# Kernel tuning notes

Measured on AMD Instinct MI355X. Metric: run time of the kernel, lower is better.

## Reference

```python
import jax, jax.numpy as jnp
import numpy as np

N = 100_000      # nodes
E = 3_200_000    # edges (avg degree 32)
HID = 64         # hid_dim == in_dim
T = 4            # S2V propagation rounds


def setup_inputs() -> dict:
    key = jax.random.key(0)
    ks = jax.random.split(key, 10)
    s = lambda fan: 1.0 / np.sqrt(fan)
    return {
        "x": jax.random.normal(ks[0], (N, HID), jnp.float32),
        "x_tag": jax.random.uniform(ks[1], (N,), jnp.float32),
        "edge_attr": jax.random.uniform(ks[2], (E, 1), jnp.float32),
        "edge_index": jax.random.randint(ks[3], (2, E), 0, N, dtype=jnp.int32),
        # per-layer bias-free Linear weights (stored as [in, out])
        "W1": jax.random.normal(ks[4], (T, HID), jnp.float32),            # lin1: 1 -> hid
        "W2": jax.random.normal(ks[5], (T, HID, HID), jnp.float32) * s(HID),  # lin2: in -> hid
        "W4": jax.random.normal(ks[6], (T, HID), jnp.float32),            # lin4: 1 -> hid
        "W5": jax.random.normal(ks[7], (2 * HID, 1), jnp.float32) * s(2 * HID),  # lin5
        "W6": jax.random.normal(ks[8], (HID, HID), jnp.float32) * s(HID),  # lin6
        "W7": jax.random.normal(ks[9], (HID, HID), jnp.float32) * s(HID),  # lin7
    }


def reference(x, x_tag, edge_attr, edge_index, W1, W2, W4, W5, W6, W7):
    src = edge_index[0]  # j (message source / p3 scatter target)
    dst = edge_index[1]  # i (aggregation target)
    for l in range(T):  # fixed small layer count
        p1 = x_tag[:, None] * W1[l][None, :]                        # lin1(x_tag)  [N,HID]
        e = jax.nn.relu(edge_attr * W4[l][None, :])                  # relu(lin4(edge_attr)) [E,HID]
        aggr = jax.ops.segment_sum(x[src], dst, num_segments=N)     # add-aggregate x_j at i
        p2 = aggr @ W2[l]                                            # lin2(aggr_out)
        p3 = jax.ops.segment_sum(e, src, num_segments=N)             # scatter_add at edge_index[0]
        x = jax.nn.relu(p1 + p2 + p3)
    graph_pool = jnp.sum(x, axis=0, keepdims=True) @ W6              # [1,HID]
    nodes_vec = x @ W7                                               # [N,HID]
    cat = jnp.concatenate(
        [jnp.broadcast_to(graph_pool, (x.shape[0], graph_pool.shape[1])), nodes_vec], axis=1
    )
    Q = jax.nn.relu(cat) @ W5                                        # [N,1]
    return Q
```

## Files before the change

### kernel.cpp

```cpp
#include <hip/hip_runtime.h>

constexpr int NN  = 100000;
constexpr int NE  = 3200000;
constexpr int HID = 64;
constexpr int TL  = 4;

constexpr int BIN_SHIFT = 9;
constexpr int BIN_NODES = 1 << BIN_SHIFT;
constexpr int NBINS     = (NN + BIN_NODES - 1) / BIN_NODES;
constexpr int BINCAP    = 18944;
constexpr int TILE_E    = 2048;

typedef unsigned short ushort_t;
typedef unsigned int uint_t;
typedef __attribute__((ext_vector_type(8))) short bf16x8;
typedef __attribute__((ext_vector_type(4))) float f32x4;

__device__ __forceinline__ ushort_t f2b(float f) {
  uint_t u = __float_as_uint(f);
  u += 0x7fff + ((u >> 16) & 1);
  return (ushort_t)(u >> 16);
}
__device__ __forceinline__ float b2f(ushort_t h) {
  return __uint_as_float(((uint_t)h) << 16);
}

__global__ __launch_bounds__(256) void escatter_kernel(
    const int* __restrict__ ei, const float* __restrict__ ea,
    int* __restrict__ bincursor, uint_t* __restrict__ gbin,
    int* __restrict__ bincursor2, uint_t* __restrict__ gbin2) {
  __shared__ int hist1[256], hist2[256];
  __shared__ int base1[NBINS], base2[NBINS];
  __shared__ int offs1[NBINS], offs2[NBINS];
  __shared__ uint_t srec[TILE_E];
  __shared__ int    sdst[TILE_E];
  int tid = threadIdx.x;
  int tb = blockIdx.x * TILE_E;
  hist1[tid] = 0; hist2[tid] = 0;
  __syncthreads();
  uint_t rec1[8], rec2[8]; int bn1[8], bn2[8], rk1[8], rk2[8];
  #pragma unroll
  for (int j = 0; j < 8; ++j) {
    int e = tb + tid + j * 256;
    bn1[j] = -1; bn2[j] = -1;
    rk1[j] = 0; rk2[j] = 0; rec1[j] = 0; rec2[j] = 0;
    if (e < NE) {
      int s = ei[e];
      int d = ei[NE + e];
      uint_t q = (uint_t)(int)(ea[e] * 8388608.0f);
      bn1[j] = d >> BIN_SHIFT;
      rec1[j] = ((uint_t)s << BIN_SHIFT) | (uint_t)(d & (BIN_NODES - 1));
      rk1[j] = atomicAdd(&hist1[bn1[j]], 1);
      bn2[j] = s >> BIN_SHIFT;
      rec2[j] = (q << BIN_SHIFT) | (uint_t)(s & (BIN_NODES - 1));
      rk2[j] = atomicAdd(&hist2[bn2[j]], 1);
    }
  }
  __syncthreads();
  int c1 = hist1[tid], c2 = hist2[tid];
  for (int o = 1; o < 256; o <<= 1) {
    int a1 = (tid >= o) ? hist1[tid - o] : 0;
    int a2 = (tid >= o) ? hist2[tid - o] : 0;
    __syncthreads();
    hist1[tid] += a1; hist2[tid] += a2;
    __syncthreads();
  }
  if (tid < NBINS) {
    offs1[tid] = hist1[tid] - c1;
    offs2[tid] = hist2[tid] - c2;
    base1[tid] = c1 ? atomicAdd(&bincursor[tid], c1) : 0;
    base2[tid] = c2 ? atomicAdd(&bincursor2[tid], c2) : 0;
  }
  __syncthreads();
  int total1 = hist1[NBINS - 1];
  int total2 = hist2[NBINS - 1];
  #pragma unroll
  for (int j = 0; j < 8; ++j) {
    if (bn1[j] >= 0) {
      int p = offs1[bn1[j]] + rk1[j];
      int gp = base1[bn1[j]] + rk1[j];
      srec[p] = rec1[j];
      sdst[p] = (gp < BINCAP) ? (bn1[j] * BINCAP + gp) : -1;
    }
  }
  __syncthreads();
  for (int t = tid; t < total1; t += 256) {
    int g = sdst[t];
    if (g >= 0) gbin[g] = srec[t];
  }
  __syncthreads();
  #pragma unroll
  for (int j = 0; j < 8; ++j) {
    if (bn2[j] >= 0) {
      int p = offs2[bn2[j]] + rk2[j];
      int gp = base2[bn2[j]] + rk2[j];
      srec[p] = rec2[j];
      sdst[p] = (gp < BINCAP) ? (bn2[j] * BINCAP + gp) : -1;
    }
  }
  __syncthreads();
  for (int t = tid; t < total2; t += 256) {
    int g = sdst[t];
    if (g >= 0) gbin2[g] = srec[t];
  }
}

__global__ __launch_bounds__(256) void binscatter_kernel(
    const int* __restrict__ ei, int* __restrict__ bincursor,
    uint_t* __restrict__ gbin) {
  __shared__ int hist[NBINS];
  __shared__ int base[NBINS];
  int tid = threadIdx.x;
  int ntiles = (NE + TILE_E - 1) / TILE_E;
  for (int tile = blockIdx.x; tile < ntiles; tile += gridDim.x) {
    int tb = tile * TILE_E;
    for (int i = tid; i < NBINS; i += 256) hist[i] = 0;
    __syncthreads();
    uint_t rec[8]; int bn[8]; int rk[8];
    #pragma unroll
    for (int j = 0; j < 8; ++j) {
      int e = tb + tid + j * 256;
      bn[j] = -1; rk[j] = 0; rec[j] = 0;
      if (e < NE) {
        int s = ei[e];
        int d = ei[NE + e];
        bn[j] = d >> BIN_SHIFT;
        rec[j] = ((uint_t)s << BIN_SHIFT) | (uint_t)(d & (BIN_NODES - 1));
        rk[j] = atomicAdd(&hist[bn[j]], 1);
      }
    }
    __syncthreads();
    for (int i = tid; i < NBINS; i += 256) {
      int c = hist[i];
      base[i] = c ? atomicAdd(&bincursor[i], c) : 0;
    }
    __syncthreads();
    #pragma unroll
    for (int j = 0; j < 8; ++j) {
      if (bn[j] >= 0) {
        int pos = base[bn[j]] + rk[j];
        if (pos < BINCAP) gbin[(size_t)bn[j] * BINCAP + pos] = rec[j];
      }
    }
    __syncthreads();
  }
}

__global__ __launch_bounds__(256) void sbinscatter_kernel(
    const int* __restrict__ ei, const float* __restrict__ ea,
    int* __restrict__ bincursor2, uint_t* __restrict__ gbin) {
  __shared__ int hist[NBINS];
  __shared__ int base[NBINS];
  int tid = threadIdx.x;
  int ntiles = (NE + TILE_E - 1) / TILE_E;
  for (int tile = blockIdx.x; tile < ntiles; tile += gridDim.x) {
    int tb = tile * TILE_E;
    for (int i = tid; i < NBINS; i += 256) hist[i] = 0;
    __syncthreads();
    uint_t rec[8]; int bn[8]; int rk[8];
    #pragma unroll
    for (int j = 0; j < 8; ++j) {
      int e = tb + tid + j * 256;
      bn[j] = -1; rk[j] = 0; rec[j] = 0;
      if (e < NE) {
        int s = ei[e];
        uint_t q = (uint_t)(int)(ea[e] * 8388608.0f);
        bn[j] = s >> BIN_SHIFT;
        rec[j] = (q << BIN_SHIFT) | (uint_t)(s & (BIN_NODES - 1));
        rk[j] = atomicAdd(&hist[bn[j]], 1);
      }
    }
    __syncthreads();
    for (int i = tid; i < NBINS; i += 256) {
      int c = hist[i];
      base[i] = c ? atomicAdd(&bincursor2[i], c) : 0;
    }
    __syncthreads();
    #pragma unroll
    for (int j = 0; j < 8; ++j) {
      if (bn[j] >= 0) {
        int pos = base[bn[j]] + rk[j];
        if (pos < BINCAP) gbin[(size_t)bn[j] * BINCAP + pos] = rec[j];
      }
    }
    __syncthreads();
  }
}

__global__ __launch_bounds__(256) void bucket_kernel(
    const uint_t* __restrict__ gbin, const int* __restrict__ bincursor,
    int* __restrict__ colidx, int* __restrict__ cnt, int cap) {
  __shared__ int cur[BIN_NODES];
  int b = blockIdx.x;
  int tid = threadIdx.x;
  for (int i = tid; i < BIN_NODES; i += 256) cur[i] = 0;
  __syncthreads();
  int cb = min(bincursor[b], BINCAP);
  const uint_t* g = gbin + (size_t)b * BINCAP;
  for (int i = tid; i < cb; i += 256) {
    uint_t r = g[i];
    int dl = (int)(r & (BIN_NODES - 1));
    int src = (int)(r >> BIN_SHIFT);
    int pos = atomicAdd(&cur[dl], 1);
    int n = (b << BIN_SHIFT) + dl;
    if (pos < cap) colidx[(size_t)n * cap + pos] = src;
  }
  __syncthreads();
  for (int i = tid; i < BIN_NODES; i += 256) {
    int n = (b << BIN_SHIFT) + i;
    if (n < NN) cnt[n] = min(cur[i], cap);
  }
  for (int gsl = tid; gsl < BIN_NODES * 64; gsl += 256) {
    int i = gsl >> 6;
    int s = gsl & 63;
    int n = (b << BIN_SHIFT) + i;
    if (n < NN && s < 48 && s >= cur[i]) colidx[(size_t)n * cap + s] = NN;
  }
}

__global__ __launch_bounds__(256) void s3bucket_kernel(
    const uint_t* __restrict__ gbin, const int* __restrict__ bincursor2,
    int* __restrict__ s3i) {
  __shared__ int acc[BIN_NODES];
  int b = blockIdx.x;
  int tid = threadIdx.x;
  for (int i = tid; i < BIN_NODES; i += 256) acc[i] = 0;
  __syncthreads();
  int cb = min(bincursor2[b], BINCAP);
  const uint_t* g = gbin + (size_t)b * BINCAP;
  for (int i = tid; i < cb; i += 256) {
    uint_t r = g[i];
    atomicAdd(&acc[r & (BIN_NODES - 1)], (int)(r >> BIN_SHIFT));
  }
  __syncthreads();
  for (int i = tid; i < BIN_NODES; i += 256) {
    int n = (b << BIN_SHIFT) + i;
    if (n < NN) s3i[n] = acc[i];
  }
}

__global__ void conv_kernel(const float* __restrict__ x, ushort_t* __restrict__ xb) {
  int i = blockIdx.x * blockDim.x + threadIdx.x;
  if (i * 4 >= NN * HID) return;
  const float4 v = *reinterpret_cast<const float4*>(&x[i * 4]);
  ushort4 o;
  o.x = f2b(v.x); o.y = f2b(v.y); o.z = f2b(v.z); o.w = f2b(v.w);
  *reinterpret_cast<ushort4*>(&xb[i * 4]) = o;
}

__global__ void wconv_kernel(const float* __restrict__ W2,
                             const float* __restrict__ W7,
                             ushort_t* __restrict__ w2t,
                             ushort_t* __restrict__ w7t) {
  int i = blockIdx.x * blockDim.x + threadIdx.x;
  int tot2 = TL * HID * HID;
  if (i < tot2) {
    int l = i >> 12, r = i & 4095, h = r >> 6, k = r & 63;
    w2t[i] = f2b(W2[(size_t)l * 4096 + k * 64 + h]);
  } else if (i < tot2 + HID * HID) {
    int j = i - tot2, h = j >> 6, k = j & 63;
    w7t[j] = f2b(W7[k * 64 + h]);
  }
}

__global__ __launch_bounds__(256) void dense_kernel(
    const ushort_t* __restrict__ xin, const ushort_t* __restrict__ wt,
    ushort_t* __restrict__ yout) {
  int lane = threadIdx.x & 63;
  int wv = (blockIdx.x * blockDim.x + threadIdx.x) >> 6;
  int n0 = wv * 32;
  if (n0 >= NN) return;
  int row = lane & 15;
  int ks = (lane >> 4) * 8;
  bf16x8 a0 = *(const bf16x8*)&xin[(size_t)(n0 + row) * HID + ks];
  bf16x8 a1 = *(const bf16x8*)&xin[(size_t)(n0 + row) * HID + 32 + ks];
  bf16x8 a2 = *(const bf16x8*)&xin[(size_t)(n0 + 16 + row) * HID + ks];
  bf16x8 a3 = *(const bf16x8*)&xin[(size_t)(n0 + 16 + row) * HID + 32 + ks];
  #pragma unroll
  for (int ct = 0; ct < 4; ++ct) {
    bf16x8 b0 = *(const bf16x8*)&wt[(ct * 16 + row) * HID + ks];
    bf16x8 b1 = *(const bf16x8*)&wt[(ct * 16 + row) * HID + 32 + ks];
    f32x4 acc0 = {0.f, 0.f, 0.f, 0.f};
    f32x4 acc1 = {0.f, 0.f, 0.f, 0.f};
    acc0 = __builtin_amdgcn_mfma_f32_16x16x32_bf16(a0, b0, acc0, 0, 0, 0);
    acc0 = __builtin_amdgcn_mfma_f32_16x16x32_bf16(a1, b1, acc0, 0, 0, 0);
    acc1 = __builtin_amdgcn_mfma_f32_16x16x32_bf16(a2, b0, acc1, 0, 0, 0);
    acc1 = __builtin_amdgcn_mfma_f32_16x16x32_bf16(a3, b1, acc1, 0, 0, 0);
    int rr = (lane >> 4) * 4;
    #pragma unroll
    for (int r = 0; r < 4; ++r) {
      yout[(size_t)(n0 + rr + r) * HID + ct * 16 + row] = f2b(acc0[r]);
      yout[(size_t)(n0 + 16 + rr + r) * HID + ct * 16 + row] = f2b(acc1[r]);
    }
  }
}

__global__ __launch_bounds__(256) void aggr_kernel(
    const ushort_t* __restrict__ yin, ushort_t* __restrict__ xout,
    const int* __restrict__ cnt, const int* __restrict__ colidx, int cap,
    const float* __restrict__ x_tag, const int* __restrict__ s3i,
    const float* __restrict__ W1l, const float* __restrict__ W4l) {
  int lane = threadIdx.x & 63;
  int wv = (blockIdx.x * blockDim.x + threadIdx.x) >> 6;
  int n0 = wv * 2;
  if (n0 >= NN) return;
  int half = lane >> 5;
  int n = n0 + half;
  int grp = (lane >> 3) & 3;
  int sub = lane & 7;
  const int* cl = colidx + (size_t)n * cap + grp;
  float f0 = 0.f, f1 = 0.f, f2 = 0.f, f3 = 0.f;
  float f4 = 0.f, f5 = 0.f, f6 = 0.f, f7 = 0.f;
  uint4 w[12];
  #pragma unroll
  for (int j = 0; j < 12; ++j) {
    int c = cl[j * 4];
    w[j] = *reinterpret_cast<const uint4*>(&yin[(size_t)c * HID + sub * 8]);
  }
  #pragma unroll
  for (int j = 0; j < 12; ++j) {
    f0 += __uint_as_float(w[j].x << 16);
    f1 += __uint_as_float(w[j].x & 0xffff0000u);
    f2 += __uint_as_float(w[j].y << 16);
    f3 += __uint_as_float(w[j].y & 0xffff0000u);
    f4 += __uint_as_float(w[j].z << 16);
    f5 += __uint_as_float(w[j].z & 0xffff0000u);
    f6 += __uint_as_float(w[j].w << 16);
    f7 += __uint_as_float(w[j].w & 0xffff0000u);
  }
  int deg = cnt[n];
  if (__any(deg > 48)) {
    int t2 = deg - 48;
    const int* ct2 = colidx + (size_t)n * cap + 48;
    for (int jt = 0; jt < 12; ++jt) {
      int idx = jt * 4 + grp;
      if (idx < t2) {
        int c = ct2[idx];
        uint4 ww = *reinterpret_cast<const uint4*>(&yin[(size_t)c * HID + sub * 8]);
        f0 += __uint_as_float(ww.x << 16);
        f1 += __uint_as_float(ww.x & 0xffff0000u);
        f2 += __uint_as_float(ww.y << 16);
        f3 += __uint_as_float(ww.y & 0xffff0000u);
        f4 += __uint_as_float(ww.z << 16);
        f5 += __uint_as_float(ww.z & 0xffff0000u);
        f6 += __uint_as_float(ww.w << 16);
        f7 += __uint_as_float(ww.w & 0xffff0000u);
      }
    }
  }
  #pragma unroll
  for (int m = 8; m <= 16; m <<= 1) {
    f0 += __shfl_xor(f0, m); f1 += __shfl_xor(f1, m);
    f2 += __shfl_xor(f2, m); f3 += __shfl_xor(f3, m);
    f4 += __shfl_xor(f4, m); f5 += __shfl_xor(f5, m);
    f6 += __shfl_xor(f6, m); f7 += __shfl_xor(f7, m);
  }
  float xt = x_tag[n];
  float s3f = (float)s3i[n] * 0x1p-23f;
  float4 w1a = *reinterpret_cast<const float4*>(&W1l[sub * 8]);
  float4 w1b = *reinterpret_cast<const float4*>(&W1l[sub * 8 + 4]);
  float4 w4a = *reinterpret_cast<const float4*>(&W4l[sub * 8]);
  float4 w4b = *reinterpret_cast<const float4*>(&W4l[sub * 8 + 4]);
  float o0 = fmaxf(fmaf(xt, w1a.x, fmaf(s3f, fmaxf(w4a.x, 0.f), f0)), 0.f);
  float o1 = fmaxf(fmaf(xt, w1a.y, fmaf(s3f, fmaxf(w4a.y, 0.f), f1)), 0.f);
  float o2 = fmaxf(fmaf(xt, w1a.z, fmaf(s3f, fmaxf(w4a.z, 0.f), f2)), 0.f);
  float o3 = fmaxf(fmaf(xt, w1a.w, fmaf(s3f, fmaxf(w4a.w, 0.f), f3)), 0.f);
  float o4 = fmaxf(fmaf(xt, w1b.x, fmaf(s3f, fmaxf(w4b.x, 0.f), f4)), 0.f);
  float o5 = fmaxf(fmaf(xt, w1b.y, fmaf(s3f, fmaxf(w4b.y, 0.f), f5)), 0.f);
  float o6 = fmaxf(fmaf(xt, w1b.z, fmaf(s3f, fmaxf(w4b.z, 0.f), f6)), 0.f);
  float o7 = fmaxf(fmaf(xt, w1b.w, fmaf(s3f, fmaxf(w4b.w, 0.f), f7)), 0.f);
  if (grp == 0) {
    uint4 o;
    o.x = (uint_t)f2b(o0) | ((uint_t)f2b(o1) << 16);
    o.y = (uint_t)f2b(o2) | ((uint_t)f2b(o3) << 16);
    o.z = (uint_t)f2b(o4) | ((uint_t)f2b(o5) << 16);
    o.w = (uint_t)f2b(o6) | ((uint_t)f2b(o7) << 16);
    *reinterpret_cast<uint4*>(&xout[(size_t)n * HID + sub * 8]) = o;
  }
}

__global__ __launch_bounds__(256) void qdense_kernel(
    const ushort_t* __restrict__ xin, const ushort_t* __restrict__ w7t,
    const float* __restrict__ w5hi, float* __restrict__ Qr,
    float* __restrict__ sumx) {
  __shared__ float ssum[4][HID];
  int tid = threadIdx.x;
  int lane = tid & 63;
  int wloc = tid >> 6;
  int wv = (blockIdx.x * blockDim.x + tid) >> 6;
  int n0 = wv * 16;
  bool valid = n0 < NN;
  int n0c = valid ? n0 : 0;
  int row = lane & 15;
  int g = lane >> 4;
  int ks = g * 8;
  bf16x8 a0 = *(const bf16x8*)&xin[(size_t)(n0c + row) * HID + ks];
  bf16x8 a1 = *(const bf16x8*)&xin[(size_t)(n0c + row) * HID + 32 + ks];
  float r0 = 0.f, r1 = 0.f, r2 = 0.f, r3 = 0.f;
  #pragma unroll
  for (int ct = 0; ct < 4; ++ct) {
    bf16x8 b0 = *(const bf16x8*)&w7t[(ct * 16 + row) * HID + ks];
    bf16x8 b1 = *(const bf16x8*)&w7t[(ct * 16 + row) * HID + 32 + ks];
    f32x4 acc = {0.f, 0.f, 0.f, 0.f};
    acc = __builtin_amdgcn_mfma_f32_16x16x32_bf16(a0, b0, acc, 0, 0, 0);
    acc = __builtin_amdgcn_mfma_f32_16x16x32_bf16(a1, b1, acc, 0, 0, 0);
    float w5 = w5hi[ct * 16 + row];
    r0 += fmaxf(acc[0], 0.f) * w5;
    r1 += fmaxf(acc[1], 0.f) * w5;
    r2 += fmaxf(acc[2], 0.f) * w5;
    r3 += fmaxf(acc[3], 0.f) * w5;
  }
  #pragma unroll
  for (int m = 1; m <= 8; m <<= 1) {
    r0 += __shfl_xor(r0, m); r1 += __shfl_xor(r1, m);
    r2 += __shfl_xor(r2, m); r3 += __shfl_xor(r3, m);
  }
  if (valid && row == 0) {
    int rb = n0 + g * 4;
    Qr[rb + 0] = r0; Qr[rb + 1] = r1; Qr[rb + 2] = r2; Qr[rb + 3] = r3;
  }
  float c[16];
  #pragma unroll
  for (int e = 0; e < 8; ++e) {
    c[e]     = valid ? b2f((ushort_t)a0[e]) : 0.f;
    c[8 + e] = valid ? b2f((ushort_t)a1[e]) : 0.f;
  }
  #pragma unroll
  for (int m = 1; m <= 8; m <<= 1) {
    #pragma unroll
    for (int e = 0; e < 16; ++e) c[e] += __shfl_xor(c[e], m);
  }
  if (row == 0) {
    #pragma unroll
    for (int e = 0; e < 8; ++e) {
      ssum[wloc][ks + e] = c[e];
      ssum[wloc][32 + ks + e] = c[8 + e];
    }
  }
  __syncthreads();
  if (tid < HID) {
    float s = ssum[0][tid] + ssum[1][tid] + ssum[2][tid] + ssum[3][tid];
    atomicAdd(&sumx[tid], s);
  }
}

__global__ void pool_kernel(const float* __restrict__ sumx, const float* __restrict__ W6,
                            const float* __restrict__ W5, float* __restrict__ c0) {
  int lane = threadIdx.x & 63;
  float sv = sumx[lane];
  float gp = 0.f;
  #pragma unroll
  for (int k = 0; k < HID; ++k) {
    float a = __int_as_float(__builtin_amdgcn_readlane(__float_as_int(sv), k));
    gp = fmaf(a, W6[k * HID + lane], gp);
  }
  float r = fmaxf(gp, 0.f) * W5[lane];
  #pragma unroll
  for (int m = 32; m >= 1; m >>= 1) r += __shfl_xor(r, m);
  if (lane == 0) *c0 = r;
}

__global__ void qfix_kernel(float* __restrict__ Q, const float* __restrict__ c0) {
  int i = blockIdx.x * blockDim.x + threadIdx.x;
  if (i < NN) Q[i] += *c0;
}

extern "C" void kernel_launch(void* const* d_in, const int* in_sizes, int n_in,
                              void* d_out, int out_size, void* d_ws, size_t ws_size,
                              hipStream_t stream) {
  const float* x         = (const float*)d_in[0];
  const float* x_tag     = (const float*)d_in[1];
  const float* edge_attr = (const float*)d_in[2];
  const int*   edge_index= (const int*)d_in[3];
  const float* W1        = (const float*)d_in[4];
  const float* W2        = (const float*)d_in[5];
  const float* W4        = (const float*)d_in[6];
  const float* W5        = (const float*)d_in[7];
  const float* W6        = (const float*)d_in[8];
  const float* W7        = (const float*)d_in[9];
  float* Q = (float*)d_out;

  const int QBLOCKS = ((NN / 16) * 64 + 255) / 256;
  const int NTILES  = (NE + TILE_E - 1) / TILE_E;

  char* ws = (char*)d_ws;
  size_t off = 0;
  auto alloc = [&](size_t bytes) -> void* {
    void* p = ws + off;
    off = (off + bytes + 255) & ~(size_t)255;
    return p;
  };
  int*      bincursor  = (int*)alloc(NBINS * 4);
  int*      bincursor2 = (int*)alloc(NBINS * 4);
  float*    sumx       = (float*)alloc(HID * 4);
  size_t zero_bytes = off;
  int*      s3i    = (int*)alloc(NN * 4);
  int*      cnt    = (int*)alloc(NN * 4);
  float*    c0     = (float*)alloc(4);
  ushort_t* xb0    = (ushort_t*)alloc((size_t)NN * HID * 2);
  ushort_t* xb1    = (ushort_t*)alloc((size_t)NN * HID * 2);
  ushort_t* ybuf   = (ushort_t*)alloc((size_t)(NN + 1) * HID * 2);
  ushort_t* w2t    = (ushort_t*)alloc((size_t)TL * HID * HID * 2);
  ushort_t* w7t    = (ushort_t*)alloc((size_t)HID * HID * 2);
  uint_t*   gbin   = (uint_t*)alloc((size_t)NBINS * BINCAP * 4);

  size_t off_nog2 = off;
  uint_t* gbin2 = (uint_t*)alloc((size_t)NBINS * BINCAP * 4);
  bool merged = true;
  {
    size_t rem = (ws_size > off) ? (ws_size - off) : 0;
    if ((int)(rem / ((size_t)NN * 4)) < 64) { merged = false; off = off_nog2; }
  }
  size_t rem = (ws_size > off) ? (ws_size - off) : 0;
  int cap = (int)(rem / ((size_t)NN * 4));
  if (cap > 96) cap = 96;
  if (cap < 64) cap = 64;
  int* colidx = (int*)alloc((size_t)NN * cap * 4);

  hipMemsetAsync(d_ws, 0, zero_bytes, stream);
  hipMemsetAsync(ybuf + (size_t)NN * HID, 0, HID * 2, stream);

  if (merged) {
    escatter_kernel<<<NTILES, 256, 0, stream>>>(edge_index, edge_attr,
                                                bincursor, gbin, bincursor2, gbin2);
    bucket_kernel<<<NBINS, 256, 0, stream>>>(gbin, bincursor, colidx, cnt, cap);
    s3bucket_kernel<<<NBINS, 256, 0, stream>>>(gbin2, bincursor2, s3i);
  } else {
    binscatter_kernel<<<NTILES, 256, 0, stream>>>(edge_index, bincursor, gbin);
    bucket_kernel<<<NBINS, 256, 0, stream>>>(gbin, bincursor, colidx, cnt, cap);
    sbinscatter_kernel<<<NTILES, 256, 0, stream>>>(edge_index, edge_attr, bincursor2, gbin);
    s3bucket_kernel<<<NBINS, 256, 0, stream>>>(gbin, bincursor2, s3i);
  }
  conv_kernel<<<(NN * HID / 4 + 255) / 256, 256, 0, stream>>>(x, xb0);
  wconv_kernel<<<((TL + 1) * HID * HID + 255) / 256, 256, 0, stream>>>(W2, W7, w2t, w7t);

  int ablocks = ((NN / 2) * 64 + 255) / 256;
  int dblocks = ((NN / 32) * 64 + 255) / 256;
  const ushort_t* xi = xb0;
  ushort_t* xo = xb1;
  for (int l = 0; l < TL; ++l) {
    dense_kernel<<<dblocks, 256, 0, stream>>>(xi, w2t + (size_t)l * HID * HID, ybuf);
    aggr_kernel<<<ablocks, 256, 0, stream>>>(ybuf, xo, cnt, colidx, cap,
                                             x_tag, s3i, W1 + l * HID, W4 + l * HID);
    ushort_t* tmp = (ushort_t*)xi;
    xi = xo;
    xo = (l == 0) ? xb0 : tmp;
  }

  qdense_kernel<<<QBLOCKS, 256, 0, stream>>>(xi, w7t, W5 + HID, Q, sumx);
  pool_kernel<<<1, 64, 0, stream>>>(sumx, W6, W5, c0);
  qfix_kernel<<<(NN + 255) / 256, 256, 0, stream>>>(Q, c0);
}
```

Measured before the change: 430.6 us.

## Fuse next-layer dense matmul into aggregation kernel and drop unmerged binning path

The aggregation kernel now takes the next layer's W2 and, after computing a 16-node tile of new features in shared memory, applies the 64x64 matmul with MFMA and writes the projected features directly. This removes the separate dense kernel launch per layer and the round trip of x through global memory. Only one dense launch is left, for layer 0. The escatter prefix scan now uses wave shuffles instead of a barrier-heavy shared-memory scan. The fallback non-merged binning path is removed, so gbin2 is always allocated, which reduces the room left for colidx when the workspace is small.

```diff
diff --git a/kernel.cpp b/kernel.cpp
--- a/kernel.cpp
+++ b/kernel.cpp
@@ -10,6 +10,8 @@
 constexpr int NBINS     = (NN + BIN_NODES - 1) / BIN_NODES;
 constexpr int BINCAP    = 18944;
 constexpr int TILE_E    = 2048;
+constexpr int PAD       = 48;
+constexpr int LROW      = 72;
 
 typedef unsigned short ushort_t;
 typedef unsigned int uint_t;
@@ -32,6 +34,7 @@
   __shared__ int hist1[256], hist2[256];
   __shared__ int base1[NBINS], base2[NBINS];
   __shared__ int offs1[NBINS], offs2[NBINS];
+  __shared__ int wt1[4], wt2[4];
   __shared__ uint_t srec[TILE_E];
   __shared__ int    sdst[TILE_E];
   int tid = threadIdx.x;
@@ -58,13 +61,20 @@
   }
   __syncthreads();
   int c1 = hist1[tid], c2 = hist2[tid];
-  for (int o = 1; o < 256; o <<= 1) {
-    int a1 = (tid >= o) ? hist1[tid - o] : 0;
-    int a2 = (tid >= o) ? hist2[tid - o] : 0;
-    __syncthreads();
-    hist1[tid] += a1; hist2[tid] += a2;
-    __syncthreads();
-  }
+  int lane = tid & 63;
+  int wvx = tid >> 6;
+  int v1 = c1, v2 = c2;
+  #pragma unroll
+  for (int o = 1; o < 64; o <<= 1) {
+    int t1 = __shfl_up(v1, o);
+    int t2 = __shfl_up(v2, o);
+    if (lane >= o) { v1 += t1; v2 += t2; }
+  }
+  if (lane == 63) { wt1[wvx] = v1; wt2[wvx] = v2; }
+  __syncthreads();
+  for (int k = 0; k < wvx; ++k) { v1 += wt1[k]; v2 += wt2[k]; }
+  hist1[tid] = v1; hist2[tid] = v2;
+  __syncthreads();
   if (tid < NBINS) {
     offs1[tid] = hist1[tid] - c1;
     offs2[tid] = hist2[tid] - c2;
@@ -102,88 +112,6 @@
   for (int t = tid; t < total2; t += 256) {
     int g = sdst[t];
     if (g >= 0) gbin2[g] = srec[t];
-  }
-}
-
-__global__ __launch_bounds__(256) void binscatter_kernel(
-    const int* __restrict__ ei, int* __restrict__ bincursor,
-    uint_t* __restrict__ gbin) {
-  __shared__ int hist[NBINS];
-  __shared__ int base[NBINS];
-  int tid = threadIdx.x;
-  int ntiles = (NE + TILE_E - 1) / TILE_E;
-  for (int tile = blockIdx.x; tile < ntiles; tile += gridDim.x) {
-    int tb = tile * TILE_E;
-    for (int i = tid; i < NBINS; i += 256) hist[i] = 0;
-    __syncthreads();
-    uint_t rec[8]; int bn[8]; int rk[8];
-    #pragma unroll
-    for (int j = 0; j < 8; ++j) {
-      int e = tb + tid + j * 256;
-      bn[j] = -1; rk[j] = 0; rec[j] = 0;
-      if (e < NE) {
-        int s = ei[e];
-        int d = ei[NE + e];
-        bn[j] = d >> BIN_SHIFT;
-        rec[j] = ((uint_t)s << BIN_SHIFT) | (uint_t)(d & (BIN_NODES - 1));
-        rk[j] = atomicAdd(&hist[bn[j]], 1);
-      }
-    }
-    __syncthreads();
-    for (int i = tid; i < NBINS; i += 256) {
-      int c = hist[i];
-      base[i] = c ? atomicAdd(&bincursor[i], c) : 0;
-    }
-    __syncthreads();
-    #pragma unroll
-    for (int j = 0; j < 8; ++j) {
-      if (bn[j] >= 0) {
-        int pos = base[bn[j]] + rk[j];
-        if (pos < BINCAP) gbin[(size_t)bn[j] * BINCAP + pos] = rec[j];
-      }
-    }
-    __syncthreads();
-  }
-}
-
-__global__ __launch_bounds__(256) void sbinscatter_kernel(
-    const int* __restrict__ ei, const float* __restrict__ ea,
-    int* __restrict__ bincursor2, uint_t* __restrict__ gbin) {
-  __shared__ int hist[NBINS];
-  __shared__ int base[NBINS];
-  int tid = threadIdx.x;
-  int ntiles = (NE + TILE_E - 1) / TILE_E;
-  for (int tile = blockIdx.x; tile < ntiles; tile += gridDim.x) {
-    int tb = tile * TILE_E;
-    for (int i = tid; i < NBINS; i += 256) hist[i] = 0;
-    __syncthreads();
-    uint_t rec[8]; int bn[8]; int rk[8];
-    #pragma unroll
-    for (int j = 0; j < 8; ++j) {
-      int e = tb + tid + j * 256;
-      bn[j] = -1; rk[j] = 0; rec[j] = 0;
-      if (e < NE) {
-        int s = ei[e];
-        uint_t q = (uint_t)(int)(ea[e] * 8388608.0f);
-        bn[j] = s >> BIN_SHIFT;
-        rec[j] = (q << BIN_SHIFT) | (uint_t)(s & (BIN_NODES - 1));
-        rk[j] = atomicAdd(&hist[bn[j]], 1);
-      }
-    }
-    __syncthreads();
-    for (int i = tid; i < NBINS; i += 256) {
-      int c = hist[i];
-      base[i] = c ? atomicAdd(&bincursor2[i], c) : 0;
-    }
-    __syncthreads();
-    #pragma unroll
-    for (int j = 0; j < 8; ++j) {
-      if (bn[j] >= 0) {
-        int pos = base[bn[j]] + rk[j];
-        if (pos < BINCAP) gbin[(size_t)bn[j] * BINCAP + pos] = rec[j];
-      }
-    }
-    __syncthreads();
   }
 }
 
@@ -214,7 +142,7 @@
     int i = gsl >> 6;
     int s = gsl & 63;
     int n = (b << BIN_SHIFT) + i;
-    if (n < NN && s < 48 && s >= cur[i]) colidx[(size_t)n * cap + s] = NN;
+    if (n < NN && s < PAD && s >= cur[i]) colidx[(size_t)n * cap + s] = NN;
   }
 }
 
@@ -295,17 +223,20 @@
   }
 }
 
-__global__ __launch_bounds__(256) void aggr_kernel(
-    const ushort_t* __restrict__ yin, ushort_t* __restrict__ xout,
+__global__ __launch_bounds__(512) void aggrf_kernel(
+    const ushort_t* __restrict__ yin, ushort_t* __restrict__ out,
+    const ushort_t* __restrict__ w2tn,
     const int* __restrict__ cnt, const int* __restrict__ colidx, int cap,
     const float* __restrict__ x_tag, const int* __restrict__ s3i,
     const float* __restrict__ W1l, const float* __restrict__ W4l) {
-  int lane = threadIdx.x & 63;
-  int wv = (blockIdx.x * blockDim.x + threadIdx.x) >> 6;
-  int n0 = wv * 2;
-  if (n0 >= NN) return;
+  __shared__ ushort_t sx[16 * LROW];
+  int tid = threadIdx.x;
+  int lane = tid & 63;
+  int wv = tid >> 6;
+  int n0b = blockIdx.x * 16;
   int half = lane >> 5;
-  int n = n0 + half;
+  int nloc = wv * 2 + half;
+  int n = n0b + nloc;
   int grp = (lane >> 3) & 3;
   int sub = lane & 7;
   const int* cl = colidx + (size_t)n * cap + grp;
@@ -329,9 +260,9 @@
     f7 += __uint_as_float(w[j].w & 0xffff0000u);
   }
   int deg = cnt[n];
-  if (__any(deg > 48)) {
-    int t2 = deg - 48;
-    const int* ct2 = colidx + (size_t)n * cap + 48;
+  if (__any(deg > PAD)) {
+    int t2 = deg - PAD;
+    const int* ct2 = colidx + (size_t)n * cap + PAD;
     for (int jt = 0; jt < 12; ++jt) {
       int idx = jt * 4 + grp;
       if (idx < t2) {
@@ -369,13 +300,34 @@
   float o5 = fmaxf(fmaf(xt, w1b.y, fmaf(s3f, fmaxf(w4b.y, 0.f), f5)), 0.f);
   float o6 = fmaxf(fmaf(xt, w1b.z, fmaf(s3f, fmaxf(w4b.z, 0.f), f6)), 0.f);
   float o7 = fmaxf(fmaf(xt, w1b.w, fmaf(s3f, fmaxf(w4b.w, 0.f), f7)), 0.f);
-  if (grp == 0) {
-    uint4 o;
-    o.x = (uint_t)f2b(o0) | ((uint_t)f2b(o1) << 16);
-    o.y = (uint_t)f2b(o2) | ((uint_t)f2b(o3) << 16);
-    o.z = (uint_t)f2b(o4) | ((uint_t)f2b(o5) << 16);
-    o.w = (uint_t)f2b(o6) | ((uint_t)f2b(o7) << 16);
-    *reinterpret_cast<uint4*>(&xout[(size_t)n * HID + sub * 8]) = o;
+  uint4 o;
+  o.x = (uint_t)f2b(o0) | ((uint_t)f2b(o1) << 16);
+  o.y = (uint_t)f2b(o2) | ((uint_t)f2b(o3) << 16);
+  o.z = (uint_t)f2b(o4) | ((uint_t)f2b(o5) << 16);
+  o.w = (uint_t)f2b(o6) | ((uint_t)f2b(o7) << 16);
+  if (w2tn) {
+    if (grp == 0)
+      *reinterpret_cast<uint4*>(&sx[nloc * LROW + sub * 8]) = o;
+    __syncthreads();
+    if (wv < 4) {
+      int row = lane & 15;
+      int ks = (lane >> 4) * 8;
+      bf16x8 a0 = *(const bf16x8*)&sx[row * LROW + ks];
+      bf16x8 a1 = *(const bf16x8*)&sx[row * LROW + 32 + ks];
+      int ct = wv;
+      bf16x8 b0 = *(const bf16x8*)&w2tn[(ct * 16 + row) * HID + ks];
+      bf16x8 b1 = *(const bf16x8*)&w2tn[(ct * 16 + row) * HID + 32 + ks];
+      f32x4 acc = {0.f, 0.f, 0.f, 0.f};
+      acc = __builtin_amdgcn_mfma_f32_16x16x32_bf16(a0, b0, acc, 0, 0, 0);
+      acc = __builtin_amdgcn_mfma_f32_16x16x32_bf16(a1, b1, acc, 0, 0, 0);
+      int rr = (lane >> 4) * 4;
+      #pragma unroll
+      for (int r = 0; r < 4; ++r)
+        out[(size_t)(n0b + rr + r) * HID + ct * 16 + row] = f2b(acc[r]);
+    }
+  } else {
+    if (grp == 0)
+      *reinterpret_cast<uint4*>(&out[(size_t)n * HID + sub * 8]) = o;
   }
 }
 
@@ -497,20 +449,14 @@
   int*      s3i    = (int*)alloc(NN * 4);
   int*      cnt    = (int*)alloc(NN * 4);
   float*    c0     = (float*)alloc(4);
-  ushort_t* xb0    = (ushort_t*)alloc((size_t)NN * HID * 2);
-  ushort_t* xb1    = (ushort_t*)alloc((size_t)NN * HID * 2);
-  ushort_t* ybuf   = (ushort_t*)alloc((size_t)(NN + 1) * HID * 2);
+  ushort_t* xf     = (ushort_t*)alloc((size_t)NN * HID * 2);
+  ushort_t* yb0    = (ushort_t*)alloc((size_t)(NN + 1) * HID * 2);
+  ushort_t* yb1    = (ushort_t*)alloc((size_t)(NN + 1) * HID * 2);
   ushort_t* w2t    = (ushort_t*)alloc((size_t)TL * HID * HID * 2);
   ushort_t* w7t    = (ushort_t*)alloc((size_t)HID * HID * 2);
   uint_t*   gbin   = (uint_t*)alloc((size_t)NBINS * BINCAP * 4);
-
-  size_t off_nog2 = off;
-  uint_t* gbin2 = (uint_t*)alloc((size_t)NBINS * BINCAP * 4);
-  bool merged = true;
-  {
-    size_t rem = (ws_size > off) ? (ws_size - off) : 0;
-    if ((int)(rem / ((size_t)NN * 4)) < 64) { merged = false; off = off_nog2; }
-  }
+  uint_t*   gbin2  = (uint_t*)alloc((size_t)NBINS * BINCAP * 4);
+
   size_t rem = (ws_size > off) ? (ws_size - off) : 0;
   int cap = (int)(rem / ((size_t)NN * 4));
   if (cap > 96) cap = 96;
@@ -518,36 +464,32 @@
   int* colidx = (int*)alloc((size_t)NN * cap * 4);
 
   hipMemsetAsync(d_ws, 0, zero_bytes, stream);
-  hipMemsetAsync(ybuf + (size_t)NN * HID, 0, HID * 2, stream);
-
-  if (merged) {
-    escatter_kernel<<<NTILES, 256, 0, stream>>>(edge_index, edge_attr,
-                                                bincursor, gbin, bincursor2, gbin2);
-    bucket_kernel<<<NBINS, 256, 0, stream>>>(gbin, bincursor, colidx, cnt, cap);
-    s3bucket_kernel<<<NBINS, 256, 0, stream>>>(gbin2, bincursor2, s3i);
-  } else {
-    binscatter_kernel<<<NTILES, 256, 0, stream>>>(edge_index, bincursor, gbin);
-    bucket_kernel<<<NBINS, 256, 0, stream>>>(gbin, bincursor, colidx, cnt, cap);
-    sbinscatter_kernel<<<NTILES, 256, 0, stream>>>(edge_index, edge_attr, bincursor2, gbin);
-    s3bucket_kernel<<<NBINS, 256, 0, stream>>>(gbin, bincursor2, s3i);
-  }
-  conv_kernel<<<(NN * HID / 4 + 255) / 256, 256, 0, stream>>>(x, xb0);
+  hipMemsetAsync(yb0 + (size_t)NN * HID, 0, HID * 2, stream);
+  hipMemsetAsync(yb1 + (size_t)NN * HID, 0, HID * 2, stream);
+
+  escatter_kernel<<<NTILES, 256, 0, stream>>>(edge_index, edge_attr,
+                                              bincursor, gbin, bincursor2, gbin2);
+  bucket_kernel<<<NBINS, 256, 0, stream>>>(gbin, bincursor, colidx, cnt, cap);
+  s3bucket_kernel<<<NBINS, 256, 0, stream>>>(gbin2, bincursor2, s3i);
+  conv_kernel<<<(NN * HID / 4 + 255) / 256, 256, 0, stream>>>(x, xf);
   wconv_kernel<<<((TL + 1) * HID * HID + 255) / 256, 256, 0, stream>>>(W2, W7, w2t, w7t);
 
-  int ablocks = ((NN / 2) * 64 + 255) / 256;
   int dblocks = ((NN / 32) * 64 + 255) / 256;
-  const ushort_t* xi = xb0;
-  ushort_t* xo = xb1;
+  dense_kernel<<<dblocks, 256, 0, stream>>>(xf, w2t, yb0);
+
+  int fblocks = NN / 16;
+  ushort_t* ycur = yb0;
+  ushort_t* ynext = yb1;
   for (int l = 0; l < TL; ++l) {
-    dense_kernel<<<dblocks, 256, 0, stream>>>(xi, w2t + (size_t)l * HID * HID, ybuf);
-    aggr_kernel<<<ablocks, 256, 0, stream>>>(ybuf, xo, cnt, colidx, cap,
-                                             x_tag, s3i, W1 + l * HID, W4 + l * HID);
-    ushort_t* tmp = (ushort_t*)xi;
-    xi = xo;
-    xo = (l == 0) ? xb0 : tmp;
-  }
-
-  qdense_kernel<<<QBLOCKS, 256, 0, stream>>>(xi, w7t, W5 + HID, Q, sumx);
+    bool last = (l == TL - 1);
+    aggrf_kernel<<<fblocks, 512, 0, stream>>>(
+        ycur, last ? xf : ynext,
+        last ? nullptr : (w2t + (size_t)(l + 1) * HID * HID),
+        cnt, colidx, cap, x_tag, s3i, W1 + l * HID, W4 + l * HID);
+    ushort_t* t = ycur; ycur = ynext; ynext = t;
+  }
+
+  qdense_kernel<<<QBLOCKS, 256, 0, stream>>>(xf, w7t, W5 + HID, Q, sumx);
   pool_kernel<<<1, 64, 0, stream>>>(sumx, W6, W5, c0);
   qfix_kernel<<<(NN + 255) / 256, 256, 0, stream>>>(Q, c0);
 }
```

Measured after the change: 410.7 us. 1.05x faster.
